# Kernel tuning notes

Hardware: AMD Instinct MI355X
Metric: run time of the kernel (lower is better)

The kernel has to match this reference:

```python
import jax, jax.numpy as jnp
import numpy as np
from jax import lax

B, L, D = 4, 4096, 1024
H = 4
DK = D // H   # head_k_dim = 256
DV = D // H   # head_v_dim = 256
HID = max(8, D // 2)  # gate trunk hidden = 512
CHUNK = 32
CONV_K = 4
EPS = 1e-5


def silu(x):
    return x * jax.nn.sigmoid(x)


def l2norm(x):
    return x * lax.rsqrt(jnp.sum(x * x, -1, keepdims=True) + 1e-6)


def causal_dwconv_silu(x, w):
    # x: (b,l,d), w: (d,k). Depthwise causal conv1d followed by SiLU (ShortConvolution).
    k = w.shape[-1]
    xp = jnp.pad(x, ((0, 0), (k - 1, 0), (0, 0))).transpose(0, 2, 1)  # (b,d,l+k-1)
    y = lax.conv_general_dilated(xp, w[:, None, :], (1,), 'VALID',
                                 feature_group_count=w.shape[0])
    return silu(y.transpose(0, 2, 1))


def delta_rule_chunkwise(q, k, v, beta, chunk=CHUNK):
    # q,k: (b,h,l,dk), v: (b,h,l,dv), beta: (b,h,l). l assumed multiple of chunk.
    b, h, l, dk = q.shape
    dv = v.shape[-1]
    n = l // chunk
    q = l2norm(q)
    k = l2norm(k)
    v = v * beta[..., None]
    kb = k * beta[..., None]
    qc = q.reshape(b, h, n, chunk, dk)
    kc = k.reshape(b, h, n, chunk, dk)
    vc = v.reshape(b, h, n, chunk, dv)
    kbc = kb.reshape(b, h, n, chunk, dk)
    # In-chunk triangular inverse: the torch loop computes (I + tril(kb k^T, -1))^{-1}
    Lm = jnp.tril(kbc @ jnp.swapaxes(kc, -1, -2), -1)  # strictly lower
    eye = jnp.eye(chunk, dtype=q.dtype)
    Tinv = jax.scipy.linalg.solve_triangular(eye + Lm, jnp.broadcast_to(eye, Lm.shape), lower=True)
    u = Tinv @ vc   # (b,h,n,c,dv)
    w = Tinv @ kbc  # (b,h,n,c,dk)
    strict = jnp.triu(jnp.ones((chunk, chunk), bool), 1)

    def step(S, inp):
        q_i, k_i, u_i, w_i = inp  # (b,h,c,d)
        attn = jnp.where(strict, 0.0, q_i @ jnp.swapaxes(k_i, -1, -2))
        u_hat = u_i - w_i @ S
        o_i = q_i @ S + attn @ u_hat
        return S + jnp.swapaxes(k_i, -1, -2) @ u_hat, o_i

    S0 = jnp.zeros((b, h, dk, dv), q.dtype)
    xs = tuple(jnp.moveaxis(t, 2, 0) for t in (qc, kc, u, w))
    S, o = lax.scan(step, S0, xs)
    o = jnp.moveaxis(o, 0, 2).reshape(b, h, l, dv)
    return o, S


def ema_rule(v, gamma):
    # v: (b,h,l,d), gamma: (b,h,l). Causal EMA: s_t = g_t*s_{t-1} + (1-g_t)*v_t
    def step(state, inp):
        v_t, g_t = inp
        state = g_t[..., None] * state + (1.0 - g_t[..., None]) * v_t
        return state, state

    s0 = jnp.zeros((v.shape[0], v.shape[1], v.shape[3]), v.dtype)
    _, out = lax.scan(step, s0, (jnp.moveaxis(v, 2, 0), jnp.moveaxis(gamma, 2, 0)))
    return jnp.moveaxis(out, 0, 2)


def hierarchical_gate(x, Wtrunk, btrunk, Wcoarse, bcoarse, Wlocal, blocal, Wglobal, bglobal, log_temp_c, log_temp_f):
    b, l, _ = x.shape
    z = silu(x @ Wtrunk.T + btrunk)  # (b,l,HID)
    tc = (jax.nn.softplus(log_temp_c) + 1e-4)[None, None, :, None]  # (1,1,h,1)
    tf = (jax.nn.softplus(log_temp_f) + 1e-4)[None, None, :, None]
    pg = jax.nn.softmax((z @ Wcoarse.T + bcoarse).reshape(b, l, H, 2) / tc, axis=-1)
    q = jax.nn.softmax((z @ Wlocal.T + blocal).reshape(b, l, H, 2) / tf, axis=-1)
    r = jax.nn.softmax((z @ Wglobal.T + bglobal).reshape(b, l, H, 2) / tf, axis=-1)
    w_v = pg[..., 0:1] * q[..., 0:1]
    w_es = pg[..., 0:1] * q[..., 1:2]
    w_d = pg[..., 1:2] * r[..., 0:1]
    w_el = pg[..., 1:2] * r[..., 1:2]
    return jnp.concatenate([w_v, w_es, w_d, w_el], axis=-1)  # (b,l,h,4)


def setup_inputs() -> dict:
    key = jax.random.key(0)
    ks = jax.random.split(key, 20)
    s = 0.02
    inp = {
        'hidden_states': jax.random.normal(ks[0], (B, L, D), jnp.float32),
        'Wq': jax.random.normal(ks[1], (D, D), jnp.float32) * s,
        'Wk': jax.random.normal(ks[2], (D, D), jnp.float32) * s,
        'Wv': jax.random.normal(ks[3], (D, D), jnp.float32) * s,
        'conv_q_w': jax.random.normal(ks[4], (D, CONV_K), jnp.float32) * 0.5,
        'conv_k_w': jax.random.normal(ks[5], (D, CONV_K), jnp.float32) * 0.5,
        'conv_v_w': jax.random.normal(ks[6], (D, CONV_K), jnp.float32) * 0.5,
        'Wb': jax.random.normal(ks[7], (H, D), jnp.float32) * s,
        'Wds': jax.random.normal(ks[8], (H, D), jnp.float32) * s,
        'bds': jnp.full((H,), -2.9444, jnp.float32),
        'Wdl': jax.random.normal(ks[9], (H, D), jnp.float32) * s,
        'bdl': jnp.full((H,), 2.9444, jnp.float32),
        'Wtrunk': jax.random.normal(ks[10], (HID, D), jnp.float32) * s,
        'btrunk': jnp.zeros((HID,), jnp.float32),
        'Wcoarse': jax.random.normal(ks[11], (H * 2, HID), jnp.float32) * s,
        'bcoarse': jnp.ones((H * 2,), jnp.float32),
        'Wlocal': jax.random.normal(ks[12], (H * 2, HID), jnp.float32) * s,
        'blocal': jnp.zeros((H * 2,), jnp.float32).at[::2].set(1.0),
        'Wglobal': jax.random.normal(ks[13], (H * 2, HID), jnp.float32) * s,
        'bglobal': jnp.zeros((H * 2,), jnp.float32).at[::2].set(1.0),
        'log_temp_c': jnp.zeros((H,), jnp.float32),  # log(1.0)
        'log_temp_f': jnp.zeros((H,), jnp.float32),
        'o_norm_w': jnp.ones((DV,), jnp.float32),
        'Wo': jax.random.normal(ks[14], (D, D), jnp.float32) * s,
    }
    return inp


def reference(hidden_states, Wq, Wk, Wv, conv_q_w, conv_k_w, conv_v_w, Wb, Wds, bds, Wdl, bdl,
              Wtrunk, btrunk, Wcoarse, bcoarse, Wlocal, blocal, Wglobal, bglobal,
              log_temp_c, log_temp_f, o_norm_w, Wo):
    x = hidden_states
    b, l, _ = x.shape
    # projections + short causal depthwise conv + SiLU
    q = causal_dwconv_silu(x @ Wq.T, conv_q_w).reshape(b, l, H, DK).transpose(0, 2, 1, 3)
    k = causal_dwconv_silu(x @ Wk.T, conv_k_w).reshape(b, l, H, DK).transpose(0, 2, 1, 3)
    v = causal_dwconv_silu(x @ Wv.T, conv_v_w).reshape(b, l, H, DV).transpose(0, 2, 1, 3)
    beta = jax.nn.sigmoid(x @ Wb.T).transpose(0, 2, 1)  # (b,h,l)
    delta_o, _ = delta_rule_chunkwise(q, k, v, beta)
    g_s = jax.nn.sigmoid(x @ Wds.T + bds).transpose(0, 2, 1)  # (b,h,l) short decay
    g_l = jax.nn.sigmoid(x @ Wdl.T + bdl).transpose(0, 2, 1)  # long decay
    ema_s = ema_rule(v, g_s)
    ema_l = ema_rule(v, g_l)
    weights = hierarchical_gate(x, Wtrunk, btrunk, Wcoarse, bcoarse, Wlocal, blocal,
                                Wglobal, bglobal, log_temp_c, log_temp_f)  # (b,l,h,4) [V,Es,D,El]
    v_b = v.transpose(0, 2, 1, 3)
    o = (weights[..., 0:1] * v_b
         + weights[..., 1:2] * ema_s.transpose(0, 2, 1, 3)
         + weights[..., 2:3] * delta_o.transpose(0, 2, 1, 3)
         + weights[..., 3:4] * ema_l.transpose(0, 2, 1, 3))
    # per-head RMSNorm
    o = o * lax.rsqrt(jnp.mean(o * o, -1, keepdims=True) + EPS) * o_norm_w
    return o.reshape(b, l, D) @ Wo.T
```

## Files before the change

kernel.cpp:

```cpp
#include <hip/hip_runtime.h>
#include <math.h>

#define BB 4
#define LL 4096
#define DD 1024
#define HH 4
#define DKk 256
#define DVv 256
#define HIDD 512
#define NC 128
#define NSEG 64
#define SEG 64

typedef unsigned short ushort_t;
typedef __attribute__((ext_vector_type(8))) short short8;
typedef __attribute__((ext_vector_type(4))) float floatx4;

__device__ __forceinline__ float sigm(float x) { return 1.f / (1.f + __expf(-x)); }

__device__ __forceinline__ float bf2f(ushort_t u) {
  union { unsigned int i; float f; } c; c.i = ((unsigned int)u) << 16; return c.f;
}
__device__ __forceinline__ ushort_t f2bf(float f) {
  union { float f; unsigned int i; } c; c.f = f;
  unsigned int lsb = (c.i >> 16) & 1u;
  return (ushort_t)((c.i + 0x7fffu + lsb) >> 16);
}
__device__ __forceinline__ void unpack2(unsigned int u, float& a, float& b) {
  union { unsigned int i; float f; } c0, c1;
  c0.i = u << 16; c1.i = u & 0xffff0000u; a = c0.f; b = c1.f;
}
__device__ __forceinline__ unsigned int pack2(float a, float b) {
  return (unsigned int)f2bf(a) | ((unsigned int)f2bf(b) << 16);
}
__device__ __forceinline__ void unpack8(const uint4 v, float* o) {
  unpack2(v.x, o[0], o[1]); unpack2(v.y, o[2], o[3]);
  unpack2(v.z, o[4], o[5]); unpack2(v.w, o[6], o[7]);
}
__device__ __forceinline__ float ubits(unsigned u) {
  union { unsigned i; float f; } c; c.i = u; return c.f;
}
__device__ __forceinline__ void split2t(float a, float b, unsigned& hi, unsigned& lo) {
  union { float f; unsigned u; } ca, cb; ca.f = a; cb.f = b;
  const unsigned ha = ca.u & 0xffff0000u, hb = cb.u & 0xffff0000u;
  hi = (ha >> 16) | hb;
  union { float f; unsigned u; } la, lb;
  la.f = a - ubits(ha); lb.f = b - ubits(hb);
  lo = (la.u >> 16) | (lb.u & 0xffff0000u);
}
__device__ __forceinline__ void gload16(const ushort_t* g, ushort_t* l) {
  __builtin_amdgcn_global_load_lds(
      (const __attribute__((address_space(1))) void*)g,
      (__attribute__((address_space(3))) void*)l, 16, 0, 0);
}

__global__ __launch_bounds__(256) void cvt_bf16_kernel(const float* __restrict__ in,
    ushort_t* __restrict__ outp, int n8)
{
  const int i = blockIdx.x * 256 + threadIdx.x;
  if (i >= n8) return;
  const float4 a = ((const float4*)in)[2*i];
  const float4 b = ((const float4*)in)[2*i + 1];
  uint4 p;
  p.x = pack2(a.x, a.y); p.y = pack2(a.z, a.w);
  p.z = pack2(b.x, b.y); p.w = pack2(b.z, b.w);
  ((uint4*)outp)[i] = p;
}

template<int ACT, int BF16OUT>
__global__ __launch_bounds__(256) void gemm_bf16(const ushort_t* __restrict__ A,
    const ushort_t* __restrict__ W, const float* __restrict__ bias,
    void* __restrict__ Cv, int M, int N, int K)
{
  __shared__ ushort_t As[128*32];
  __shared__ ushort_t Ws[128*32];
  const int tid = threadIdx.x;
  const int bm = blockIdx.y * 128, bn = blockIdx.x * 128;
  const int lane = tid & 63, wave = tid >> 6;
  const int wm = (wave >> 1) * 64, wn = (wave & 1) * 64;
  const int fr = lane & 15, fq = lane >> 4;
  const int srow = wave * 16 + (lane >> 2);
  const int scol = (lane & 3) * 8;
  const ushort_t* Ap = A + (size_t)(bm + srow) * K + scol;
  const ushort_t* Wp = W + (size_t)(bn + srow) * K + scol;
  ushort_t* AsD = &As[wave * 512];
  ushort_t* WsD = &Ws[wave * 512];
  floatx4 acc[4][4];
#pragma unroll
  for (int i = 0; i < 4; ++i)
#pragma unroll
    for (int j = 0; j < 4; ++j) acc[i][j] = (floatx4){0.f, 0.f, 0.f, 0.f};

  for (int k0 = 0; k0 < K; k0 += 32) {
    __syncthreads();
    gload16(Ap + k0, AsD);
    gload16(Ap + (size_t)64 * K + k0, AsD + 64*32);
    gload16(Wp + k0, WsD);
    gload16(Wp + (size_t)64 * K + k0, WsD + 64*32);
    __syncthreads();
    short8 af[4], bf_[4];
#pragma unroll
    for (int mt = 0; mt < 4; ++mt)
      af[mt] = *(const short8*)&As[(wm + mt*16 + fr)*32 + fq*8];
#pragma unroll
    for (int nt = 0; nt < 4; ++nt)
      bf_[nt] = *(const short8*)&Ws[(wn + nt*16 + fr)*32 + fq*8];
#pragma unroll
    for (int mt = 0; mt < 4; ++mt)
#pragma unroll
      for (int nt = 0; nt < 4; ++nt)
        acc[mt][nt] = __builtin_amdgcn_mfma_f32_16x16x32_bf16(af[mt], bf_[nt], acc[mt][nt], 0, 0, 0);
  }
#pragma unroll
  for (int mt = 0; mt < 4; ++mt) {
#pragma unroll
    for (int reg = 0; reg < 4; ++reg) {
      const int row = bm + wm + mt*16 + fq*4 + reg;
#pragma unroll
      for (int nt = 0; nt < 4; ++nt) {
        const int col = bn + wn + nt*16 + fr;
        float v = acc[mt][nt][reg];
        if (ACT == 1) { v += bias[col]; v = v * sigm(v); }
        if (BF16OUT) ((ushort_t*)Cv)[(size_t)row * N + col] = f2bf(v);
        else         ((float*)Cv)[(size_t)row * N + col] = v;
      }
    }
  }
}

__global__ __launch_bounds__(256) void conv_silu_kernel(const ushort_t* __restrict__ xin,
    const float* __restrict__ wc, ushort_t* __restrict__ outp)
{
  const size_t idx = (size_t)blockIdx.x * 256 + threadIdx.x;
  const int d = (int)(idx & (DD - 1));
  const int l = (int)((idx >> 10) & (LL - 1));
  const float4 w = *(const float4*)(wc + d * 4);
  const ushort_t* xp = xin + idx;
  float acc = w.w * bf2f(xp[0]);
  if (l >= 1) acc += w.z * bf2f(xp[-DD]);
  if (l >= 2) acc += w.y * bf2f(xp[-2*DD]);
  if (l >= 3) acc += w.x * bf2f(xp[-3*DD]);
  acc = acc * sigm(acc);
  const int b = (int)(idx >> 22);
  const int h = d >> 8, dk = d & 255;
  outp[(((size_t)(b*HH + h))*LL + l)*DKk + dk] = f2bf(acc);
}

__global__ __launch_bounds__(256) void small_proj_kernel(const float* __restrict__ x,
   const float* __restrict__ Wb, const float* __restrict__ Wds, const float* __restrict__ bds,
   const float* __restrict__ Wdl, const float* __restrict__ bdl,
   float* __restrict__ beta, float* __restrict__ gs, float* __restrict__ gl)
{
  const int bl = blockIdx.x;
  const int t = threadIdx.x, wave = t >> 6, lane = t & 63;
  __shared__ float res[12];
  const float* xr = x + (size_t)bl * DD + lane * 16;
  const float4 x0 = *(const float4*)(xr);
  const float4 x1 = *(const float4*)(xr + 4);
  const float4 x2 = *(const float4*)(xr + 8);
  const float4 x3 = *(const float4*)(xr + 12);
  for (int rr = 0; rr < 3; ++rr) {
    const int r = wave * 3 + rr;
    const int mat = r >> 2, h = r & 3;
    const float* Wr = (mat == 0 ? Wb : (mat == 1 ? Wds : Wdl)) + (size_t)h * DD + lane * 16;
    const float4 w0 = *(const float4*)(Wr);
    const float4 w1 = *(const float4*)(Wr + 4);
    const float4 w2 = *(const float4*)(Wr + 8);
    const float4 w3 = *(const float4*)(Wr + 12);
    float p = x0.x*w0.x + x0.y*w0.y + x0.z*w0.z + x0.w*w0.w
            + x1.x*w1.x + x1.y*w1.y + x1.z*w1.z + x1.w*w1.w
            + x2.x*w2.x + x2.y*w2.y + x2.z*w2.z + x2.w*w2.w
            + x3.x*w3.x + x3.y*w3.y + x3.z*w3.z + x3.w*w3.w;
#pragma unroll
    for (int o = 1; o < 64; o <<= 1) p += __shfl_xor(p, o);
    if (lane == 0) res[r] = p;
  }
  __syncthreads();
  if (t < 12) {
    const int mat = t >> 2, h = t & 3;
    float v = res[t];
    if (mat == 1) v += bds[h];
    if (mat == 2) v += bdl[h];
    v = sigm(v);
    const int b = bl >> 12, l = bl & (LL - 1);
    const size_t o = ((size_t)(b*HH + h))*LL + l;
    (mat == 0 ? beta : (mat == 1 ? gs : gl))[o] = v;
  }
}

__global__ __launch_bounds__(256) void gate_kernel(const ushort_t* __restrict__ z,
  const float* __restrict__ Wc, const float* __restrict__ bc,
  const float* __restrict__ Wl, const float* __restrict__ bl_,
  const float* __restrict__ Wg, const float* __restrict__ bg,
  const float* __restrict__ ltc, const float* __restrict__ ltf,
  float* __restrict__ wgt)
{
  const int bl = blockIdx.x;
  const int t = threadIdx.x, wave = t >> 6, lane = t & 63;
  __shared__ float res[24];
  const uint4 zv = *(const uint4*)(z + (size_t)bl * HIDD + lane * 8);
  float zf[8]; unpack8(zv, zf);
  for (int rr = 0; rr < 6; ++rr) {
    const int r = wave * 6 + rr;
    const int mat = r >> 3, qi = r & 7;
    const float* Wr = (mat == 0 ? Wc : (mat == 1 ? Wl : Wg)) + (size_t)qi * HIDD + lane * 8;
    const float4 w0 = *(const float4*)(Wr);
    const float4 w1 = *(const float4*)(Wr + 4);
    float p = zf[0]*w0.x + zf[1]*w0.y + zf[2]*w0.z + zf[3]*w0.w
            + zf[4]*w1.x + zf[5]*w1.y + zf[6]*w1.z + zf[7]*w1.w;
#pragma unroll
    for (int o = 1; o < 64; o <<= 1) p += __shfl_xor(p, o);
    if (lane == 0) {
      const float* br = (mat == 0 ? bc : (mat == 1 ? bl_ : bg));
      res[r] = p + br[qi];
    }
  }
  __syncthreads();
  if (t < 4) {
    const float tc = logf(1.f + __expf(ltc[t])) + 1e-4f;
    const float tf = logf(1.f + __expf(ltf[t])) + 1e-4f;
    const float pg0 = sigm((res[2*t]     - res[2*t+1])     / tc);
    const float q0  = sigm((res[8+2*t]   - res[8+2*t+1])   / tf);
    const float r0  = sigm((res[16+2*t]  - res[16+2*t+1])  / tf);
    float* o = wgt + ((size_t)bl * HH + t) * 4;
    o[0] = pg0 * q0;         o[1] = pg0 * (1.f - q0);
    o[2] = (1.f - pg0) * r0; o[3] = (1.f - pg0) * (1.f - r0);
  }
}

#define QS 264
__global__ __launch_bounds__(256) void prep_kernel(ushort_t* __restrict__ q,
    ushort_t* __restrict__ k, const ushort_t* __restrict__ v,
    const float* __restrict__ beta,
    ushort_t* __restrict__ u, ushort_t* __restrict__ w,
    ushort_t* __restrict__ ah, ushort_t* __restrict__ al)
{
  __shared__ ushort_t qb[32*QS];
  __shared__ ushort_t kb[32*QS];
  __shared__ float Lm[32*32];
  __shared__ float betas[32];
  const int bid = blockIdx.x;
  const int ci = bid & (NC - 1);
  const int bh = bid >> 7;
  const int t = threadIdx.x;
  const size_t base = ((size_t)bh * LL + ci*32) * DKk;
  if (t < 32) betas[t] = beta[(size_t)bh * LL + ci*32 + t];
  for (int i4 = t; i4 < 1024; i4 += 256) {
    const int r = i4 >> 5, e = (i4 & 31) * 8;
    *(uint4*)&qb[r*QS + e] = *(const uint4*)(q + base + r*256 + e);
    *(uint4*)&kb[r*QS + e] = *(const uint4*)(k + base + r*256 + e);
  }
  __syncthreads();
  {
    const int r = t >> 3, g = t & 7;
    float sq = 0.f, sk = 0.f;
    for (int e = g*32; e < g*32 + 32; ++e) {
      const float a = bf2f(qb[r*QS + e]); sq = fmaf(a, a, sq);
      const float c = bf2f(kb[r*QS + e]); sk = fmaf(c, c, sk);
    }
#pragma unroll
    for (int o = 1; o < 8; o <<= 1) { sq += __shfl_xor(sq, o); sk += __shfl_xor(sk, o); }
    const float rq = rsqrtf(sq + 1e-6f), rk = rsqrtf(sk + 1e-6f);
    for (int e = g*32; e < g*32 + 32; ++e) {
      qb[r*QS + e] = f2bf(bf2f(qb[r*QS + e]) * rq);
      kb[r*QS + e] = f2bf(bf2f(kb[r*QS + e]) * rk);
    }
  }
  __syncthreads();
  for (int i4 = t; i4 < 1024; i4 += 256) {
    const int r = i4 >> 5, e = (i4 & 31) * 8;
    *(uint4*)(q + base + r*256 + e) = *(const uint4*)&qb[r*QS + e];
  }
  {
    unsigned int pk[16];
#pragma unroll
    for (int j = 0; j < 16; ++j)
      pk[j] = (unsigned int)kb[(2*j)*QS + t] | ((unsigned int)kb[(2*j+1)*QS + t] << 16);
    uint4* kd = (uint4*)(k + base + (size_t)t*32);
#pragma unroll
    for (int j = 0; j < 4; ++j) kd[j] = ((const uint4*)pk)[j];
  }
  {
    const int j = t & 31, i0 = (t >> 5) * 4;
#pragma unroll
    for (int ii = 0; ii < 4; ++ii) {
      const int i = i0 + ii;
      float dq = 0.f, dk2 = 0.f;
      for (int e = 0; e < 256; ++e) {
        const float kj = bf2f(kb[j*QS + e]);
        dq  = fmaf(bf2f(qb[i*QS + e]), kj, dq);
        dk2 = fmaf(bf2f(kb[i*QS + e]), kj, dk2);
      }
      const float av = (j <= i) ? dq : 0.f;
      const ushort_t hh = f2bf(av);
      const size_t aoff = ((size_t)bh*NC + ci)*1024 + (size_t)i*32 + j;
      ah[aoff] = hh;
      al[aoff] = f2bf(av - bf2f(hh));
      Lm[i*32 + j] = (j < i) ? betas[i] * dk2 : 0.f;
    }
  }
  __syncthreads();
  {
    float cu[32], cw[32];
#pragma unroll
    for (int r = 0; r < 32; ++r) {
      cu[r] = bf2f(v[base + r*256 + t]) * betas[r];
      cw[r] = bf2f(kb[r*QS + t]) * betas[r];
    }
#pragma unroll
    for (int i = 1; i < 32; ++i) {
      float au = cu[i], aw = cw[i];
#pragma unroll
      for (int j = 0; j < i; ++j) {
        const float lm = Lm[i*32 + j];
        au = fmaf(-lm, cu[j], au);
        aw = fmaf(-lm, cw[j], aw);
      }
      cu[i] = au; cw[i] = aw;
    }
    {
      unsigned int pu[16];
#pragma unroll
      for (int j = 0; j < 16; ++j) pu[j] = pack2(cu[2*j], cu[2*j+1]);
      uint4* ud = (uint4*)(u + base + (size_t)t*32);
#pragma unroll
      for (int j = 0; j < 4; ++j) ud[j] = ((const uint4*)pu)[j];
    }
#pragma unroll
    for (int r = 0; r < 32; ++r) w[base + r*256 + t] = f2bf(cw[r]);
  }
}

#define S16(dv,kk) (((dv)<<8) + ((kk) ^ (((dv)&7)<<3)))
#define U16(dv,cr) (((dv)<<5) + ((cr) ^ (((dv)&3)<<3)))

__global__ __launch_bounds__(256, 1) void scan_kernel(
    const ushort_t* __restrict__ qn, const ushort_t* __restrict__ kt,
    const ushort_t* __restrict__ ut, const ushort_t* __restrict__ w,
    const ushort_t* __restrict__ ah, const ushort_t* __restrict__ al,
    float* __restrict__ dout)
{
  __shared__ ushort_t STh[16*256];
  __shared__ ushort_t STl[16*256];
  __shared__ ushort_t Uh[16*32];
  __shared__ ushort_t Ul[16*32];
  const int bid = blockIdx.x;
  const int bh = bid & 15, vs = bid >> 4;
  const int b = bh >> 2, h = bh & 3;
  const int t = threadIdx.x, lane = t & 63, wv = t >> 6;
  const int fr = lane & 15, fq = lane >> 4;
  const int mt = wv & 1;
  const bool isW = (wv < 2);

  for (int i = t; i < 512; i += 256) {
    ((uint4*)STh)[i] = (uint4){0u,0u,0u,0u};
    ((uint4*)STl)[i] = (uint4){0u,0u,0u,0u};
  }

  const size_t bhL = (size_t)bh * LL;
  const ushort_t* wqB = (isW ? w : qn) + bhL * DKk;
  const ushort_t* kB  = kt + bhL * DKk;
  const ushort_t* uB  = ut + bhL * DVv;
  const ushort_t* ahB = ah + (size_t)bh * NC * 1024;
  const ushort_t* alB = al + (size_t)bh * NC * 1024;
  float* oB = dout + (size_t)b * LL * DD + h * DVv + vs * 16 + fr;

  floatx4 Sacc[4];
#pragma unroll
  for (int i = 0; i < 4; ++i) Sacc[i] = (floatx4){0.f,0.f,0.f,0.f};

  short8 aw[8]; uint2 uu;
  auto loadA = [&](int ci) {
    const ushort_t* ap = wqB + (size_t)(ci*32 + mt*16 + fr) * DKk + fq*8;
#pragma unroll
    for (int ks = 0; ks < 8; ++ks) aw[ks] = *(const short8*)(ap + ks*32);
    if (isW)
      uu = *(const uint2*)(uB + (size_t)ci*8192 + (size_t)(vs*16 + fr)*32 + mt*16 + fq*4);
  };

  loadA(0);
  __syncthreads();

  for (int ci = 0; ci < NC; ++ci) {
    short8 kf[4];
    {
      const ushort_t* kp = kB + (size_t)ci*8192 + (size_t)(wv*64 + fr)*32 + fq*8;
#pragma unroll
      for (int m = 0; m < 4; ++m) kf[m] = *(const short8*)(kp + m*512);
    }
    short8 afh, afl;
    if (!isW) {
      afh = *(const short8*)(ahB + (size_t)ci*1024 + (mt*16+fr)*32 + fq*8);
      afl = *(const short8*)(alB + (size_t)ci*1024 + (mt*16+fr)*32 + fq*8);
    }
    floatx4 acc0, acc1;
    if (isW) {
      float u0,u1,u2,u3; unpack2(uu.x,u0,u1); unpack2(uu.y,u2,u3);
      acc0 = (floatx4){-u0,-u1,-u2,-u3};
      acc1 = (floatx4){0.f,0.f,0.f,0.f};
#pragma unroll
      for (int ks = 0; ks < 8; ++ks) {
        const short8 sh = *(const short8*)&STh[S16(fr, ks*32 + fq*8)];
        const short8 sl = *(const short8*)&STl[S16(fr, ks*32 + fq*8)];
        acc0 = __builtin_amdgcn_mfma_f32_16x16x32_bf16(aw[ks], sh, acc0, 0,0,0);
        acc1 = __builtin_amdgcn_mfma_f32_16x16x32_bf16(aw[ks], sl, acc1, 0,0,0);
      }
      const float v0 = -(acc0[0]+acc1[0]), v1 = -(acc0[1]+acc1[1]);
      const float v2 = -(acc0[2]+acc1[2]), v3 = -(acc0[3]+acc1[3]);
      unsigned ph0, pl0, ph1, pl1;
      split2t(v0, v1, ph0, pl0); split2t(v2, v3, ph1, pl1);
      *(uint2*)&Uh[U16(fr, mt*16 + fq*4)] = (uint2){ph0, ph1};
      *(uint2*)&Ul[U16(fr, mt*16 + fq*4)] = (uint2){pl0, pl1};
    } else {
      acc0 = (floatx4){0.f,0.f,0.f,0.f};
#pragma unroll
      for (int ks = 0; ks < 8; ++ks) {
        const short8 sh = *(const short8*)&STh[S16(fr, ks*32 + fq*8)];
        acc0 = __builtin_amdgcn_mfma_f32_16x16x32_bf16(aw[ks], sh, acc0, 0,0,0);
      }
    }
    __syncthreads();
    if (ci + 1 < NC) loadA(ci + 1);
    const short8 uhh = *(const short8*)&Uh[U16(fr, fq*8)];
    const short8 uhl = *(const short8*)&Ul[U16(fr, fq*8)];
    if (!isW) {
      acc0 = __builtin_amdgcn_mfma_f32_16x16x32_bf16(afh, uhh, acc0, 0,0,0);
      acc0 = __builtin_amdgcn_mfma_f32_16x16x32_bf16(afh, uhl, acc0, 0,0,0);
      acc0 = __builtin_amdgcn_mfma_f32_16x16x32_bf16(afl, uhh, acc0, 0,0,0);
      float* op = oB + (size_t)(ci*32 + mt*16 + fq*4) * DD;
#pragma unroll
      for (int r = 0; r < 4; ++r) op[(size_t)r * DD] = acc0[r];
    }
#pragma unroll
    for (int m = 0; m < 4; ++m) {
      Sacc[m] = __builtin_amdgcn_mfma_f32_16x16x32_bf16(kf[m], uhh, Sacc[m], 0,0,0);
      Sacc[m] = __builtin_amdgcn_mfma_f32_16x16x32_bf16(kf[m], uhl, Sacc[m], 0,0,0);
    }
#pragma unroll
    for (int m = 0; m < 4; ++m) {
      unsigned ph0, pl0, ph1, pl1;
      split2t(Sacc[m][0], Sacc[m][1], ph0, pl0);
      split2t(Sacc[m][2], Sacc[m][3], ph1, pl1);
      const int dk0 = wv*64 + m*16 + fq*4;
      *(uint2*)&STh[S16(fr, dk0)] = (uint2){ph0, ph1};
      *(uint2*)&STl[S16(fr, dk0)] = (uint2){pl0, pl1};
    }
    __syncthreads();
  }
}

__global__ __launch_bounds__(256) void ema_local_kernel(const ushort_t* __restrict__ v,
  const float* __restrict__ gs, const float* __restrict__ gl,
  ushort_t* __restrict__ es, ushort_t* __restrict__ el,
  float* __restrict__ Bs, float* __restrict__ Bl,
  float* __restrict__ As, float* __restrict__ Al,
  float* __restrict__ PfS, float* __restrict__ PfL)
{
  const int bid = blockIdx.x;
  const int seg = bid & (NSEG - 1), bh = bid >> 6;
  const int b = bh >> 2, h = bh & 3;
  const int dv = threadIdx.x;
  const int l0 = seg * SEG;
  const ushort_t* vp = v + ((size_t)bh*LL + l0) * DVv + dv;
  const float* gsp = gs + (size_t)bh*LL + l0;
  const float* glp = gl + (size_t)bh*LL + l0;
  ushort_t* esp = es + ((size_t)b*LL + l0)*DD + h*DVv + dv;
  ushort_t* elp = el + ((size_t)b*LL + l0)*DD + h*DVv + dv;
  float* pfs = PfS + (size_t)bh*LL + l0;
  float* pfl = PfL + (size_t)bh*LL + l0;
  float s1 = 0.f, s2 = 0.f, p1 = 1.f, p2 = 1.f;
  for (int j = 0; j < SEG; ++j) {
    const float vv = bf2f(vp[(size_t)j * DVv]);
    const float a = gsp[j], g2 = glp[j];
    s1 = fmaf(a,  s1, (1.f - a)  * vv);
    s2 = fmaf(g2, s2, (1.f - g2) * vv);
    p1 *= a; p2 *= g2;
    esp[(size_t)j * DD] = f2bf(s1);
    elp[(size_t)j * DD] = f2bf(s2);
    if (dv == 0) { pfs[j] = p1; pfl[j] = p2; }
  }
  const size_t o = (((size_t)bh*NSEG + seg) << 8) + dv;
  Bs[o] = s1; Bl[o] = s2;
  if (dv == 0) { As[bh*NSEG + seg] = p1; Al[bh*NSEG + seg] = p2; }
}

__global__ __launch_bounds__(256) void ema_carry_kernel(
  const float* __restrict__ Bs, const float* __restrict__ Bl,
  const float* __restrict__ As, const float* __restrict__ Al,
  float* __restrict__ Cs, float* __restrict__ Cl)
{
  const int bh = blockIdx.x;
  const int dv = threadIdx.x;
  __shared__ float Ash[NSEG], Alh[NSEG];
  if (dv < NSEG) { Ash[dv] = As[bh*NSEG + dv]; Alh[dv] = Al[bh*NSEG + dv]; }
  __syncthreads();
  float c1 = 0.f, c2 = 0.f;
  for (int s = 0; s < NSEG; ++s) {
    const size_t o = (((size_t)bh*NSEG + s) << 8) + dv;
    Cs[o] = c1; Cl[o] = c2;
    c1 = fmaf(Ash[s], c1, Bs[o]);
    c2 = fmaf(Alh[s], c2, Bl[o]);
  }
}

__global__ __launch_bounds__(64) void combine_kernel(const ushort_t* __restrict__ v,
  const ushort_t* __restrict__ es, const ushort_t* __restrict__ el,
  const float* __restrict__ dov, const float* __restrict__ wgt,
  const float* __restrict__ onw,
  const float* __restrict__ Cs, const float* __restrict__ Cl,
  const float* __restrict__ PfS, const float* __restrict__ PfL,
  ushort_t* __restrict__ outp)
{
  const int bid = blockIdx.x;
  const int h = bid & 3;
  const size_t bl = (size_t)(bid >> 2);
  const int lane = threadIdx.x;
  const size_t b = bl >> 12;
  const size_t l = bl & (LL - 1);
  const int bh = (int)(b * HH) + h;
  const int seg = (int)(l >> 6);
  const size_t vidx = (((b*HH + h) * (size_t)LL) + l) * DVv + lane*4;
  const size_t didx = bl * DD + h*DVv + lane*4;
  const uint2 vu = *(const uint2*)(v + vidx);
  const uint2 eu = *(const uint2*)(es + didx);
  const uint2 gu = *(const uint2*)(el + didx);
  const float4 d4 = *(const float4*)(dov + didx);
  const float pS = PfS[(size_t)bh*LL + l];
  const float pL = PfL[(size_t)bh*LL + l];
  const float4 cs4 = *(const float4*)(Cs + (((size_t)bh*NSEG + seg) << 8) + lane*4);
  const float4 cl4 = *(const float4*)(Cl + (((size_t)bh*NSEG + seg) << 8) + lane*4);
  float vf[4], ef[4], gf[4];
  unpack2(vu.x, vf[0], vf[1]); unpack2(vu.y, vf[2], vf[3]);
  unpack2(eu.x, ef[0], ef[1]); unpack2(eu.y, ef[2], ef[3]);
  unpack2(gu.x, gf[0], gf[1]); unpack2(gu.y, gf[2], gf[3]);
  ef[0] = fmaf(pS, cs4.x, ef[0]); ef[1] = fmaf(pS, cs4.y, ef[1]);
  ef[2] = fmaf(pS, cs4.z, ef[2]); ef[3] = fmaf(pS, cs4.w, ef[3]);
  gf[0] = fmaf(pL, cl4.x, gf[0]); gf[1] = fmaf(pL, cl4.y, gf[1]);
  gf[2] = fmaf(pL, cl4.z, gf[2]); gf[3] = fmaf(pL, cl4.w, gf[3]);
  const float* wp = wgt + (size_t)bid * 4;
  const float w0 = wp[0], w1 = wp[1], w2 = wp[2], w3 = wp[3];
  float o[4];
  const float df[4] = {d4.x, d4.y, d4.z, d4.w};
  float ss = 0.f;
#pragma unroll
  for (int i = 0; i < 4; ++i) {
    o[i] = w0*vf[i] + w1*ef[i] + w2*df[i] + w3*gf[i];
    ss = fmaf(o[i], o[i], ss);
  }
#pragma unroll
  for (int off = 1; off < 64; off <<= 1) ss += __shfl_xor(ss, off);
  const float sc = rsqrtf(ss * (1.f / DVv) + 1e-5f);
  const float4 nw = *(const float4*)(onw + lane*4);
  uint2 pk;
  pk.x = pack2(o[0]*sc*nw.x, o[1]*sc*nw.y);
  pk.y = pack2(o[2]*sc*nw.z, o[3]*sc*nw.w);
  *(uint2*)(outp + didx) = pk;
}

extern "C" void kernel_launch(void* const* d_in, const int* in_sizes, int n_in,
                              void* d_out, int out_size, void* d_ws, size_t ws_size,
                              hipStream_t stream)
{
  const float* x    = (const float*)d_in[0];
  const float* Wq   = (const float*)d_in[1];
  const float* Wk   = (const float*)d_in[2];
  const float* Wv   = (const float*)d_in[3];
  const float* cqw  = (const float*)d_in[4];
  const float* ckw  = (const float*)d_in[5];
  const float* cvw  = (const float*)d_in[6];
  const float* Wb   = (const float*)d_in[7];
  const float* Wds  = (const float*)d_in[8];
  const float* bds  = (const float*)d_in[9];
  const float* Wdl  = (const float*)d_in[10];
  const float* bdl  = (const float*)d_in[11];
  const float* Wtr  = (const float*)d_in[12];
  const float* btr  = (const float*)d_in[13];
  const float* Wc   = (const float*)d_in[14];
  const float* bc   = (const float*)d_in[15];
  const float* Wl   = (const float*)d_in[16];
  const float* blc  = (const float*)d_in[17];
  const float* Wg   = (const float*)d_in[18];
  const float* bg   = (const float*)d_in[19];
  const float* ltc  = (const float*)d_in[20];
  const float* ltf  = (const float*)d_in[21];
  const float* onw  = (const float*)d_in[22];
  const float* Wo   = (const float*)d_in[23];
  float* outp = (float*)d_out;

  const size_t BLD = (size_t)BB * LL * DD;
  unsigned char* w8 = (unsigned char*)d_ws;
  const size_t SL = BLD * 2;
  ushort_t* SA = (ushort_t*)(w8 + 0*SL);
  ushort_t* SB = (ushort_t*)(w8 + 1*SL);
  ushort_t* SC = (ushort_t*)(w8 + 2*SL);
  ushort_t* SD = (ushort_t*)(w8 + 3*SL);
  ushort_t* SE = (ushort_t*)(w8 + 4*SL);
  ushort_t* zb   = (ushort_t*)(w8 + 5*SL);
  ushort_t* attn_hi = (ushort_t*)(w8 + 5*SL + BLD);
  ushort_t* attn_lo = attn_hi + (size_t)BB*HH*NC*1024;
  float*    beta = (float*)(attn_hi + 2*(size_t)BB*HH*NC*1024);
  float*    gs   = beta + (size_t)BB*HH*LL;
  float*    gl   = gs   + (size_t)BB*HH*LL;
  float*    wgt  = gl   + (size_t)BB*HH*LL;
  float*    Bs   = wgt  + (size_t)BB*LL*HH*4;
  float*    Bl   = Bs   + (size_t)BB*HH*NSEG*256;
  float*    Cs   = Bl   + (size_t)BB*HH*NSEG*256;
  float*    Cl   = Cs   + (size_t)BB*HH*NSEG*256;
  float*    As   = Cl   + (size_t)BB*HH*NSEG*256;
  float*    Al   = As   + (size_t)BB*HH*NSEG;
  float*    PfS  = Al   + (size_t)BB*HH*NSEG;
  float*    PfL  = PfS  + (size_t)BB*HH*LL;
  ushort_t* Wqb  = (ushort_t*)(PfL + (size_t)BB*HH*LL);
  ushort_t* Wkb  = Wqb + (size_t)DD*DD;
  ushort_t* Wvb  = Wkb + (size_t)DD*DD;
  ushort_t* Wob  = Wvb + (size_t)DD*DD;
  ushort_t* Wtrb = Wob + (size_t)DD*DD;
  ushort_t* xb   = SD;
  float*    dov  = outp;

  const int MBL = BB * LL;
  dim3 blk256(256);

  cvt_bf16_kernel<<<dim3((unsigned)(BLD/8/256)), blk256, 0, stream>>>(x, xb, (int)(BLD/8));
  cvt_bf16_kernel<<<dim3(DD*DD/8/256), blk256, 0, stream>>>(Wq, Wqb, DD*DD/8);
  cvt_bf16_kernel<<<dim3(DD*DD/8/256), blk256, 0, stream>>>(Wk, Wkb, DD*DD/8);
  cvt_bf16_kernel<<<dim3(DD*DD/8/256), blk256, 0, stream>>>(Wv, Wvb, DD*DD/8);
  cvt_bf16_kernel<<<dim3(DD*DD/8/256), blk256, 0, stream>>>(Wo, Wob, DD*DD/8);
  cvt_bf16_kernel<<<dim3(HIDD*DD/8/256), blk256, 0, stream>>>(Wtr, Wtrb, HIDD*DD/8);

  gemm_bf16<0,1><<<dim3(DD/128, MBL/128), blk256, 0, stream>>>(xb, Wqb, nullptr, SA, MBL, DD, DD);
  gemm_bf16<0,1><<<dim3(DD/128, MBL/128), blk256, 0, stream>>>(xb, Wkb, nullptr, SB, MBL, DD, DD);
  gemm_bf16<0,1><<<dim3(DD/128, MBL/128), blk256, 0, stream>>>(xb, Wvb, nullptr, SC, MBL, DD, DD);
  gemm_bf16<1,1><<<dim3(HIDD/128, MBL/128), blk256, 0, stream>>>(xb, Wtrb, btr, zb, MBL, HIDD, DD);
  small_proj_kernel<<<dim3(MBL), blk256, 0, stream>>>(x, Wb, Wds, bds, Wdl, bdl, beta, gs, gl);
  gate_kernel<<<dim3(MBL), blk256, 0, stream>>>(zb, Wc, bc, Wl, blc, Wg, bg, ltc, ltf, wgt);
  conv_silu_kernel<<<dim3((unsigned)(BB*LL*DD/256)), blk256, 0, stream>>>(SA, cqw, SD);
  conv_silu_kernel<<<dim3((unsigned)(BB*LL*DD/256)), blk256, 0, stream>>>(SB, ckw, SA);
  conv_silu_kernel<<<dim3((unsigned)(BB*LL*DD/256)), blk256, 0, stream>>>(SC, cvw, SB);
  prep_kernel<<<dim3(BB*HH*NC), blk256, 0, stream>>>(SD, SA, SB, beta, SC, SE, attn_hi, attn_lo);
  scan_kernel<<<dim3(256), blk256, 0, stream>>>(SD, SA, SC, SE, attn_hi, attn_lo, dov);
  ema_local_kernel<<<dim3(BB*HH*NSEG), blk256, 0, stream>>>(SB, gs, gl, SE, SD, Bs, Bl, As, Al, PfS, PfL);
  ema_carry_kernel<<<dim3(BB*HH), blk256, 0, stream>>>(Bs, Bl, As, Al, Cs, Cl);
  combine_kernel<<<dim3(MBL*HH), dim3(64), 0, stream>>>(SB, SE, SD, dov, wgt, onw, Cs, Cl, PfS, PfL, SA);
  gemm_bf16<0,0><<<dim3(DD/128, MBL/128), blk256, 0, stream>>>(SA, Wob, nullptr, outp, MBL, DD, DD);
}
```

Baseline: 1.127 ms.

## Vectorize conv, use MFMA for prep dot products, split scan over more blocks

The depthwise conv+SiLU kernel now handles 8 channels per thread with 128-bit loads and stores, which cuts the thread count and memory transactions. The prep kernel's 32x32 in-chunk q·k and k·k dot products move from a scalar 256-length loop to bf16 MFMA tiles. The sequential scan kernel goes from 256 to 512 blocks, each owning 8 value columns instead of 16, with launch bounds raised to 2 blocks per CU. The aim is more parallelism in the latency-bound scan, at the cost of half the MFMA lanes doing redundant work on duplicated U columns.

```diff
diff --git a/kernel.cpp b/kernel.cpp
--- a/kernel.cpp
+++ b/kernel.cpp
@@ -131,19 +131,36 @@
 __global__ __launch_bounds__(256) void conv_silu_kernel(const ushort_t* __restrict__ xin,
     const float* __restrict__ wc, ushort_t* __restrict__ outp)
 {
-  const size_t idx = (size_t)blockIdx.x * 256 + threadIdx.x;
-  const int d = (int)(idx & (DD - 1));
-  const int l = (int)((idx >> 10) & (LL - 1));
-  const float4 w = *(const float4*)(wc + d * 4);
-  const ushort_t* xp = xin + idx;
-  float acc = w.w * bf2f(xp[0]);
-  if (l >= 1) acc += w.z * bf2f(xp[-DD]);
-  if (l >= 2) acc += w.y * bf2f(xp[-2*DD]);
-  if (l >= 3) acc += w.x * bf2f(xp[-3*DD]);
-  acc = acc * sigm(acc);
-  const int b = (int)(idx >> 22);
-  const int h = d >> 8, dk = d & 255;
-  outp[(((size_t)(b*HH + h))*LL + l)*DKk + dk] = f2bf(acc);
+  const size_t i8 = (size_t)blockIdx.x * 256 + threadIdx.x;
+  const int d8 = (int)((i8 & 127) << 3);
+  const int l  = (int)((i8 >> 7) & (LL - 1));
+  const int b  = (int)(i8 >> 19);
+  const ushort_t* xp = xin + i8 * 8;
+  const uint4 z4 = (uint4){0u,0u,0u,0u};
+  const uint4 v0 = *(const uint4*)xp;
+  const uint4 v1 = (l >= 1) ? *(const uint4*)(xp - DD)   : z4;
+  const uint4 v2 = (l >= 2) ? *(const uint4*)(xp - 2*DD) : z4;
+  const uint4 v3 = (l >= 3) ? *(const uint4*)(xp - 3*DD) : z4;
+  float x0[8], x1[8], x2[8], x3[8];
+  unpack8(v0, x0); unpack8(v1, x1); unpack8(v2, x2); unpack8(v3, x3);
+  unsigned pk[4];
+#pragma unroll
+  for (int p = 0; p < 4; ++p) {
+    float o2[2];
+#pragma unroll
+    for (int q = 0; q < 2; ++q) {
+      const int j = p*2 + q;
+      const float4 w = *(const float4*)(wc + (d8 + j) * 4);
+      float acc = w.w * x0[j];
+      acc = fmaf(w.z, x1[j], acc);
+      acc = fmaf(w.y, x2[j], acc);
+      acc = fmaf(w.x, x3[j], acc);
+      o2[q] = acc * sigm(acc);
+    }
+    pk[p] = pack2(o2[0], o2[1]);
+  }
+  const int h = d8 >> 8, dk = d8 & 255;
+  *(uint4*)(outp + (((size_t)(b*HH + h))*LL + l)*DKk + dk) = *(uint4*)pk;
 }
 
 __global__ __launch_bounds__(256) void small_proj_kernel(const float* __restrict__ x,
@@ -281,22 +298,29 @@
     for (int j = 0; j < 4; ++j) kd[j] = ((const uint4*)pk)[j];
   }
   {
-    const int j = t & 31, i0 = (t >> 5) * 4;
-#pragma unroll
-    for (int ii = 0; ii < 4; ++ii) {
-      const int i = i0 + ii;
-      float dq = 0.f, dk2 = 0.f;
-      for (int e = 0; e < 256; ++e) {
-        const float kj = bf2f(kb[j*QS + e]);
-        dq  = fmaf(bf2f(qb[i*QS + e]), kj, dq);
-        dk2 = fmaf(bf2f(kb[i*QS + e]), kj, dk2);
-      }
-      const float av = (j <= i) ? dq : 0.f;
+    const int lane = t & 63, wv4 = t >> 6;
+    const int fr = lane & 15, fq = lane >> 4;
+    const int it = wv4 >> 1, jt = wv4 & 1;
+    floatx4 dq = (floatx4){0.f,0.f,0.f,0.f};
+    floatx4 dk2 = (floatx4){0.f,0.f,0.f,0.f};
+#pragma unroll
+    for (int ks = 0; ks < 8; ++ks) {
+      const short8 bfk = *(const short8*)&kb[(jt*16+fr)*QS + ks*32 + fq*8];
+      const short8 afq = *(const short8*)&qb[(it*16+fr)*QS + ks*32 + fq*8];
+      const short8 afk = *(const short8*)&kb[(it*16+fr)*QS + ks*32 + fq*8];
+      dq  = __builtin_amdgcn_mfma_f32_16x16x32_bf16(afq, bfk, dq, 0,0,0);
+      dk2 = __builtin_amdgcn_mfma_f32_16x16x32_bf16(afk, bfk, dk2, 0,0,0);
+    }
+#pragma unroll
+    for (int reg = 0; reg < 4; ++reg) {
+      const int i = it*16 + fq*4 + reg;
+      const int j = jt*16 + fr;
+      const float av = (j <= i) ? dq[reg] : 0.f;
       const ushort_t hh = f2bf(av);
       const size_t aoff = ((size_t)bh*NC + ci)*1024 + (size_t)i*32 + j;
       ah[aoff] = hh;
       al[aoff] = f2bf(av - bf2f(hh));
-      Lm[i*32 + j] = (j < i) ? betas[i] * dk2 : 0.f;
+      Lm[i*32 + j] = (j < i) ? betas[i] * dk2[reg] : 0.f;
     }
   }
   __syncthreads();
@@ -334,7 +358,7 @@
 #define S16(dv,kk) (((dv)<<8) + ((kk) ^ (((dv)&7)<<3)))
 #define U16(dv,cr) (((dv)<<5) + ((cr) ^ (((dv)&3)<<3)))
 
-__global__ __launch_bounds__(256, 1) void scan_kernel(
+__global__ __launch_bounds__(256, 2) void scan_kernel(
     const ushort_t* __restrict__ qn, const ushort_t* __restrict__ kt,
     const ushort_t* __restrict__ ut, const ushort_t* __restrict__ w,
     const ushort_t* __restrict__ ah, const ushort_t* __restrict__ al,
@@ -363,7 +387,7 @@
   const ushort_t* uB  = ut + bhL * DVv;
   const ushort_t* ahB = ah + (size_t)bh * NC * 1024;
   const ushort_t* alB = al + (size_t)bh * NC * 1024;
-  float* oB = dout + (size_t)b * LL * DD + h * DVv + vs * 16 + fr;
+  float* oB = dout + (size_t)b * LL * DD + h * DVv + vs * 8 + fr;
 
   floatx4 Sacc[4];
 #pragma unroll
@@ -375,7 +399,7 @@
 #pragma unroll
     for (int ks = 0; ks < 8; ++ks) aw[ks] = *(const short8*)(ap + ks*32);
     if (isW)
-      uu = *(const uint2*)(uB + (size_t)ci*8192 + (size_t)(vs*16 + fr)*32 + mt*16 + fq*4);
+      uu = *(const uint2*)(uB + (size_t)ci*8192 + (size_t)(vs*8 + (fr & 7))*32 + mt*16 + fq*4);
   };
 
   loadA(0);
@@ -427,9 +451,11 @@
       acc0 = __builtin_amdgcn_mfma_f32_16x16x32_bf16(afh, uhh, acc0, 0,0,0);
       acc0 = __builtin_amdgcn_mfma_f32_16x16x32_bf16(afh, uhl, acc0, 0,0,0);
       acc0 = __builtin_amdgcn_mfma_f32_16x16x32_bf16(afl, uhh, acc0, 0,0,0);
-      float* op = oB + (size_t)(ci*32 + mt*16 + fq*4) * DD;
-#pragma unroll
-      for (int r = 0; r < 4; ++r) op[(size_t)r * DD] = acc0[r];
+      if (fr < 8) {
+        float* op = oB + (size_t)(ci*32 + mt*16 + fq*4) * DD;
+#pragma unroll
+        for (int r = 0; r < 4; ++r) op[(size_t)r * DD] = acc0[r];
+      }
     }
 #pragma unroll
     for (int m = 0; m < 4; ++m) {
@@ -634,11 +660,11 @@
   gemm_bf16<1,1><<<dim3(HIDD/128, MBL/128), blk256, 0, stream>>>(xb, Wtrb, btr, zb, MBL, HIDD, DD);
   small_proj_kernel<<<dim3(MBL), blk256, 0, stream>>>(x, Wb, Wds, bds, Wdl, bdl, beta, gs, gl);
   gate_kernel<<<dim3(MBL), blk256, 0, stream>>>(zb, Wc, bc, Wl, blc, Wg, bg, ltc, ltf, wgt);
-  conv_silu_kernel<<<dim3((unsigned)(BB*LL*DD/256)), blk256, 0, stream>>>(SA, cqw, SD);
-  conv_silu_kernel<<<dim3((unsigned)(BB*LL*DD/256)), blk256, 0, stream>>>(SB, ckw, SA);
-  conv_silu_kernel<<<dim3((unsigned)(BB*LL*DD/256)), blk256, 0, stream>>>(SC, cvw, SB);
+  conv_silu_kernel<<<dim3((unsigned)(BLD/8/256)), blk256, 0, stream>>>(SA, cqw, SD);
+  conv_silu_kernel<<<dim3((unsigned)(BLD/8/256)), blk256, 0, stream>>>(SB, ckw, SA);
+  conv_silu_kernel<<<dim3((unsigned)(BLD/8/256)), blk256, 0, stream>>>(SC, cvw, SB);
   prep_kernel<<<dim3(BB*HH*NC), blk256, 0, stream>>>(SD, SA, SB, beta, SC, SE, attn_hi, attn_lo);
-  scan_kernel<<<dim3(256), blk256, 0, stream>>>(SD, SA, SC, SE, attn_hi, attn_lo, dov);
+  scan_kernel<<<dim3(512), blk256, 0, stream>>>(SD, SA, SC, SE, attn_hi, attn_lo, dov);
   ema_local_kernel<<<dim3(BB*HH*NSEG), blk256, 0, stream>>>(SB, gs, gl, SE, SD, Bs, Bl, As, Al, PfS, PfL);
   ema_carry_kernel<<<dim3(BB*HH), blk256, 0, stream>>>(Bs, Bl, As, Al, Cs, Cl);
   combine_kernel<<<dim3(MBL*HH), dim3(64), 0, stream>>>(SB, SE, SD, dov, wgt, onw, Cs, Cl, PfS, PfL, SA);
```

Result: no change. 1.145 ms (+1.7%).
